# Performance work log

Measured on AMD Instinct MI355X. Metric: run time of the kernel, lower is better.

## Reference

```python
import jax, jax.numpy as jnp
import numpy as np

EMB = 16
L = 100
B = 8192
BN_EPS = 1e-5


def _bn(x, g, b):
    # BatchNorm1d in training mode: biased batch stats over dim 0. x: [b, EMB]
    mu = jnp.mean(x, axis=0)
    var = jnp.mean((x - mu) ** 2, axis=0)
    return g * (x - mu) / jnp.sqrt(var + BN_EPS) + b


def _pool(me, aw, g6, b6, a6):
    # me: [b, L, EMB] masked embeddings; aw: [b, L, 1] masked attention logits
    s = jnp.sum(me, axis=1)                       # sum pool
    mean = jnp.mean(me, axis=1)                   # mean over full L (incl. padding), as in torch
    sq = me * me
    l2 = jnp.sum(sq, axis=-1)                     # [b, L]
    mx_i = jnp.argmax(l2, axis=1)                 # first max, matches torch.max
    mn_i = jnp.argmin(jnp.where(l2 == 0, jnp.asarray(9999.0, l2.dtype), l2), axis=1)
    mx = jnp.take_along_axis(me, mx_i[:, None, None], axis=1)[:, 0]
    mn = jnp.take_along_axis(me, mn_i[:, None, None], axis=1)[:, 0]
    attw = jax.nn.softmax(aw, axis=1)             # softmax over L incl. zeroed pads (faithful)
    at = jnp.sum(me * attw, axis=1)
    ko = 0.5 * (s * s - jnp.sum(sq, axis=1))      # korder (FM-style)
    ko = ko / jnp.maximum(jnp.linalg.norm(ko, axis=-1, keepdims=True), 1e-12)
    # branch order: sum, mean, max, min, korder, atten (matches torch.cat order)
    pools = jnp.stack([
        _bn(s, g6[0], b6[0]), _bn(mean, g6[1], b6[1]), _bn(mx, g6[2], b6[2]),
        _bn(mn, g6[3], b6[3]), _bn(ko, g6[4], b6[4]), _bn(at, g6[5], b6[5])], axis=1)
    w = jax.nn.softmax(a6)[None, :, None]
    return jnp.sum(pools * w, axis=1)             # [b, EMB]


def setup_inputs() -> dict:
    key = jax.random.key(0)
    ks = jax.random.split(key, 24)
    f32 = jnp.float32
    inp = {
        'uid': jax.random.randint(ks[0], (B,), 0, 139000),
        'mid': jax.random.randint(ks[1], (B,), 0, 132000),
        'yr': jax.random.randint(ks[2], (B,), 0, 150),
        'ids_ug': jax.random.randint(ks[3], (B, L), 0, 30),
        'ids_urb': jax.random.randint(ks[4], (B, L), 0, 132000),
        'ids_mg': jax.random.randint(ks[5], (B, L), 0, 30),
        'ids_mt': jax.random.randint(ks[6], (B, L), 0, 41000),
        'len_ug': jax.random.randint(ks[7], (B,), 1, L + 1),
        'len_urb': jax.random.randint(ks[8], (B,), 1, L + 1),
        'len_mg': jax.random.randint(ks[9], (B,), 1, L + 1),
        'len_mt': jax.random.randint(ks[10], (B,), 1, L + 1),
        'emb_userId': jax.random.normal(ks[11], (139000, EMB), f32) * 0.05,
        'emb_movieId': jax.random.normal(ks[12], (132000, EMB), f32) * 0.05,
        'emb_tagId': jax.random.normal(ks[13], (41000, EMB), f32) * 0.05,
        'emb_genreId': jax.random.normal(ks[14], (30, EMB), f32) * 0.05,
        'emb_year': jax.random.normal(ks[15], (150, EMB), f32) * 0.05,
        # init_param(): atten embeddings ~ N(1.0, 1e-6)
        'att_movieId': 1.0 + jax.random.normal(ks[16], (132000, 1), f32) * 1e-6,
        'att_tagId': 1.0 + jax.random.normal(ks[17], (41000, 1), f32) * 1e-6,
        'att_genreId': 1.0 + jax.random.normal(ks[18], (30, 1), f32) * 1e-6,
        'bn_gamma': jnp.ones((4, 6, EMB), f32),
        'bn_beta': jnp.zeros((4, 6, EMB), f32),
        'alpha': jnp.ones((4, 6), f32),
        'W1': jax.random.normal(ks[19], (112, 64), f32) * 0.05,
        'b1': jnp.zeros((64,), f32),
        'W2': jax.random.normal(ks[20], (64, 32), f32) * 0.05,
        'b2': jnp.zeros((32,), f32),
        'W3': jax.random.normal(ks[21], (32, 1), f32) * 0.05,
        'b3': jnp.zeros((1,), f32),
    }
    return inp


def reference(uid, mid, yr, ids_ug, ids_urb, ids_mg, ids_mt,
              len_ug, len_urb, len_mg, len_mt,
              emb_userId, emb_movieId, emb_tagId, emb_genreId, emb_year,
              att_movieId, att_tagId, att_genreId,
              bn_gamma, bn_beta, alpha, W1, b1, W2, b2, W3, b3):
    emb1 = jnp.concatenate([emb_userId[uid], emb_movieId[mid], emb_year[yr]], axis=1)  # [b, 48]
    ar = jnp.arange(L)
    fields = [
        (ids_ug, len_ug, emb_genreId, att_genreId),
        (ids_urb, len_urb, emb_movieId, att_movieId),
        (ids_mg, len_mg, emb_genreId, att_genreId),
        (ids_mt, len_mt, emb_tagId, att_tagId),
    ]
    pooled = []
    for i, (ids, ln, tab, atab) in enumerate(fields):
        m = (ln[:, None] > ar)[..., None].astype(tab.dtype)  # [b, L, 1]
        me = tab[ids] * m
        aw = atab[ids] * m
        pooled.append(_pool(me, aw, bn_gamma[i], bn_beta[i], alpha[i]))
    x = jnp.concatenate([emb1] + pooled, axis=1)  # [b, 112]
    h = jax.nn.relu(x @ W1 + b1)
    h = jax.nn.relu(h @ W2 + b2)
    return jax.nn.sigmoid(h @ W3 + b3)[:, 0]
```

## Files before the change

kernel.cpp:

```cpp
#include <hip/hip_runtime.h>
#include <math.h>

#define BATCH 8192
#define L 100
#define EMB 16
#define NCH 384
#define NG  512

#define POOLED_FLOATS (4 * BATCH * 96)
#define POOLED_BYTES  (POOLED_FLOATS * 4)
#define PART_FLOATS   (NCH * NG)

__global__ __launch_bounds__(256) void pool_kernel(
    const int* __restrict__ ids_ug, const int* __restrict__ ids_urb,
    const int* __restrict__ ids_mg, const int* __restrict__ ids_mt,
    const int* __restrict__ len_ug, const int* __restrict__ len_urb,
    const int* __restrict__ len_mg, const int* __restrict__ len_mt,
    const float* __restrict__ emb_movie, const float* __restrict__ emb_tag,
    const float* __restrict__ emb_genre,
    const float* __restrict__ att_movie, const float* __restrict__ att_tag,
    const float* __restrict__ att_genre,
    float* __restrict__ pooled, float* __restrict__ psum, float* __restrict__ psq)
{
    const int bx  = blockIdx.x;
    const int f   = bx & 3;
    const int g   = bx >> 2;
    const int tid = threadIdx.x;
    const int sub = tid >> 4;
    const int e   = tid & 15;
    const int j   = e >> 2;
    const int c   = e & 3;
    const int b   = g * 16 + sub;

    const int* ids; const int* lens; const float* tab; const float* atab;
    switch (f) {
        case 0: ids = ids_ug;  lens = len_ug;  tab = emb_genre; atab = att_genre; break;
        case 1: ids = ids_urb; lens = len_urb; tab = emb_movie; atab = att_movie; break;
        case 2: ids = ids_mg;  lens = len_mg;  tab = emb_genre; atab = att_genre; break;
        default:ids = ids_mt;  lens = len_mt;  tab = emb_tag;   atab = att_tag;   break;
    }
    const int ln = lens[b];
    const float4* __restrict__ tab4 = (const float4*)tab;

    __shared__ float tile[16][100];
    __shared__ int   sids[16 * 100];
    __shared__ float gtab[480];
    __shared__ float gexp[32];

    {
        const int4* idsrc = (const int4*)(ids + (size_t)g * (16 * L));
        ((int4*)sids)[tid]       = idsrc[tid];
        if (tid < 144) ((int4*)sids)[256 + tid] = idsrc[256 + tid];
    }
    const bool genre = (f == 0) | (f == 2);
    if (genre) {
        for (int i = tid; i < 480; i += 256) gtab[i] = emb_genre[i];
        if (tid < 30) gexp[tid] = __expf(att_genre[tid]);
    }
    __syncthreads();
    const int* idrow = &sids[sub * 100];

    float4 s   = make_float4(0.f, 0.f, 0.f, 0.f);
    float4 ssq = s, att = s, mxv = s, mnv = s;
    float expsum = 0.f;
    float bestmx = -1e30f; int lx = 0x7fffffff;
    float bestmn =  1e30f; int lm = 0x7fffffff;

    auto ACC = [&](const float4 v, const float ew, const int l) {
        float4 v2;
        v2.x = v.x * v.x; v2.y = v.y * v.y; v2.z = v.z * v.z; v2.w = v.w * v.w;
        s.x += v.x; s.y += v.y; s.z += v.z; s.w += v.w;
        ssq.x += v2.x; ssq.y += v2.y; ssq.z += v2.z; ssq.w += v2.w;
        float pl2 = (v2.x + v2.y) + (v2.z + v2.w);
        float l2 = pl2 + __shfl_xor(pl2, 1);
        l2 += __shfl_xor(l2, 2);
        if (l2 > bestmx) { bestmx = l2; lx = l; mxv = v; }
        float l2m = (l2 == 0.0f) ? 9999.0f : l2;
        if (l2m < bestmn) { bestmn = l2m; lm = l; mnv = v; }
        expsum += ew;
        att.x += v.x * ew; att.y += v.y * ew; att.z += v.z * ew; att.w += v.w * ew;
    };

    if (!genre) {
        int l = j;
        if (l < ln) {
            int id0 = idrow[l];
            float4 v0 = tab4[(size_t)id0 * 4 + c];
            float aw0 = atab[id0];
            while (l + 4 < ln) {
                const int id1 = idrow[l + 4];
                float4 v1 = tab4[(size_t)id1 * 4 + c];
                float aw1 = atab[id1];
                ACC(v0, __expf(aw0), l);
                v0 = v1; aw0 = aw1; l += 4;
            }
            ACC(v0, __expf(aw0), l);
        }
    } else {
        for (int l = j; l < ln; l += 4) {
            const int id = idrow[l];
            float4 v = *(const float4*)&gtab[id * 16 + c * 4];
            ACC(v, gexp[id], l);
        }
    }

    #pragma unroll
    for (int m = 4; m <= 8; m <<= 1) {
        float obx = __shfl_xor(bestmx, m);
        int   olx = __shfl_xor(lx, m);
        float ax = __shfl_xor(mxv.x, m), ay = __shfl_xor(mxv.y, m);
        float az = __shfl_xor(mxv.z, m), aw2 = __shfl_xor(mxv.w, m);
        if (obx > bestmx || (obx == bestmx && olx < lx)) {
            bestmx = obx; lx = olx; mxv = make_float4(ax, ay, az, aw2);
        }
        float obn = __shfl_xor(bestmn, m);
        int   olm = __shfl_xor(lm, m);
        float bx2 = __shfl_xor(mnv.x, m), by = __shfl_xor(mnv.y, m);
        float bz  = __shfl_xor(mnv.z, m), bw = __shfl_xor(mnv.w, m);
        if (obn < bestmn || (obn == bestmn && olm < lm)) {
            bestmn = obn; lm = olm; mnv = make_float4(bx2, by, bz, bw);
        }
        s.x += __shfl_xor(s.x, m); s.y += __shfl_xor(s.y, m);
        s.z += __shfl_xor(s.z, m); s.w += __shfl_xor(s.w, m);
        ssq.x += __shfl_xor(ssq.x, m); ssq.y += __shfl_xor(ssq.y, m);
        ssq.z += __shfl_xor(ssq.z, m); ssq.w += __shfl_xor(ssq.w, m);
        att.x += __shfl_xor(att.x, m); att.y += __shfl_xor(att.y, m);
        att.z += __shfl_xor(att.z, m); att.w += __shfl_xor(att.w, m);
        expsum += __shfl_xor(expsum, m);
    }
    expsum += (float)(L - ln);

    float4 mean;
    mean.x = s.x * (1.0f / L); mean.y = s.y * (1.0f / L);
    mean.z = s.z * (1.0f / L); mean.w = s.w * (1.0f / L);
    float4 ko;
    ko.x = 0.5f * (s.x * s.x - ssq.x); ko.y = 0.5f * (s.y * s.y - ssq.y);
    ko.z = 0.5f * (s.z * s.z - ssq.z); ko.w = 0.5f * (s.w * s.w - ssq.w);
    float pk = (ko.x * ko.x + ko.y * ko.y) + (ko.z * ko.z + ko.w * ko.w);
    float kn2 = pk + __shfl_xor(pk, 1);
    kn2 += __shfl_xor(kn2, 2);
    float rn = 1.0f / fmaxf(sqrtf(kn2), 1e-12f);
    ko.x *= rn; ko.y *= rn; ko.z *= rn; ko.w *= rn;
    float ie = 1.0f / expsum;
    att.x *= ie; att.y *= ie; att.z *= ie; att.w *= ie;

    float4 pv[6] = { s, mean, mxv, mnv, ko, att };

    float4* prow = (float4*)(pooled + ((size_t)(f * BATCH + b)) * 96);
    if (j == 0) {
        #pragma unroll
        for (int p = 0; p < 6; ++p) {
            prow[p * 4 + c] = pv[p];
            *(float4*)&tile[sub][p * 16 + c * 4] = pv[p];
        }
    }
    __syncthreads();
    if (tid < 96) {
        float sm = 0.f, sq = 0.f;
        #pragma unroll
        for (int s2 = 0; s2 < 16; ++s2) {
            float x = tile[s2][tid];
            sm += x;
            sq += x * x;
        }
        psum[(size_t)(f * 96 + tid) * NG + g] = sm;
        psq [(size_t)(f * 96 + tid) * NG + g] = sq;
    }
}

__global__ __launch_bounds__(256) void coef_kernel(
    const float* __restrict__ psum, const float* __restrict__ psq,
    const float* __restrict__ gamma, const float* __restrict__ beta,
    const float* __restrict__ alpha,
    float* __restrict__ coefA, float* __restrict__ coefB)
{
    const int tid   = threadIdx.x;
    const int chl   = tid >> 3;
    const int strip = tid & 7;
    const int ch    = blockIdx.x * 32 + chl;
    const float4* ps = (const float4*)(psum + (size_t)ch * NG + strip * 64);
    const float4* pq = (const float4*)(psq  + (size_t)ch * NG + strip * 64);
    double dsm = 0.0, dsq = 0.0;
    #pragma unroll
    for (int i = 0; i < 16; ++i) {
        float4 a = ps[i];
        dsm += ((double)a.x + (double)a.y) + ((double)a.z + (double)a.w);
        float4 bq = pq[i];
        dsq += ((double)bq.x + (double)bq.y) + ((double)bq.z + (double)bq.w);
    }
    #pragma unroll
    for (int m = 1; m <= 4; m <<= 1) {
        dsm += __shfl_xor(dsm, m);
        dsq += __shfl_xor(dsq, m);
    }
    if (strip == 0) {
        const int f = ch / 96;
        const int p = (ch % 96) >> 4;
        double mu  = dsm * (1.0 / BATCH);
        double var = dsq * (1.0 / BATCH) - mu * mu;
        float inv = (float)(1.0 / sqrt(var + 1e-5));
        float gm = gamma[ch];
        float bb = beta[ch];
        float amax = -1e30f;
        for (int q = 0; q < 6; ++q) amax = fmaxf(amax, alpha[f * 6 + q]);
        float wsum = 0.f;
        for (int q = 0; q < 6; ++q) wsum += __expf(alpha[f * 6 + q] - amax);
        float wp = __expf(alpha[f * 6 + p] - amax) / wsum;
        coefA[ch] = wp * gm * inv;
        coefB[ch] = wp * (bb - gm * (float)mu * inv);
    }
}

#define SPB 16
__global__ __launch_bounds__(256) void final_kernel(
    const int* __restrict__ uid, const int* __restrict__ mid, const int* __restrict__ yr,
    const float* __restrict__ emb_user, const float* __restrict__ emb_movie,
    const float* __restrict__ emb_year,
    const float* __restrict__ pooled,
    const float* __restrict__ coefA, const float* __restrict__ coefB,
    const float* __restrict__ W1, const float* __restrict__ b1,
    const float* __restrict__ W2, const float* __restrict__ b2,
    const float* __restrict__ W3, const float* __restrict__ b3,
    float* __restrict__ out)
{
    __shared__ float sW1[112 * 64];
    __shared__ float sW2[64 * 32];
    __shared__ float sW3[32];
    __shared__ float sb1[64];
    __shared__ float sb2[32];
    __shared__ float xt[SPB][112];
    __shared__ float h1t[SPB][64];

    const int tid = threadIdx.x;
    for (int i = tid; i < 112 * 16; i += 256)
        ((float4*)sW1)[i] = ((const float4*)W1)[i];
    for (int i = tid; i < 64 * 8; i += 256)
        ((float4*)sW2)[i] = ((const float4*)W2)[i];
    if (tid < 32) sW3[tid] = W3[tid];
    if (tid < 64) sb1[tid] = b1[tid];
    if (tid < 32) sb2[tid] = b2[tid];

    const int sub = tid >> 4;
    const int e   = tid & 15;
    const int b   = blockIdx.x * SPB + sub;

    xt[sub][e]      = emb_user [(size_t)uid[b] * EMB + e];
    xt[sub][16 + e] = emb_movie[(size_t)mid[b] * EMB + e];
    xt[sub][32 + e] = emb_year [(size_t)yr[b]  * EMB + e];

    #pragma unroll
    for (int f = 0; f < 4; ++f) {
        const float* pr = pooled + ((size_t)(f * BATCH + b)) * 96;
        float acc = 0.f;
        #pragma unroll
        for (int p = 0; p < 6; ++p) {
            int c = f * 96 + p * 16 + e;
            acc += coefA[c] * pr[p * 16 + e] + coefB[c];
        }
        xt[sub][48 + f * 16 + e] = acc;
    }
    __syncthreads();

    float4 h1 = ((float4*)sb1)[e];
    for (int k = 0; k < 112; ++k) {
        float xk = xt[sub][k];
        float4 w = ((float4*)sW1)[k * 16 + e];
        h1.x += xk * w.x; h1.y += xk * w.y; h1.z += xk * w.z; h1.w += xk * w.w;
    }
    float4 h1r;
    h1r.x = fmaxf(h1.x, 0.f); h1r.y = fmaxf(h1.y, 0.f);
    h1r.z = fmaxf(h1.z, 0.f); h1r.w = fmaxf(h1.w, 0.f);
    *(float4*)&h1t[sub][e * 4] = h1r;
    __syncthreads();

    float2 h2 = ((float2*)sb2)[e];
    for (int k = 0; k < 64; ++k) {
        float hk = h1t[sub][k];
        float2 w = ((float2*)sW2)[k * 16 + e];
        h2.x += hk * w.x; h2.y += hk * w.y;
    }
    float part = fmaxf(h2.x, 0.f) * sW3[2 * e] + fmaxf(h2.y, 0.f) * sW3[2 * e + 1];
    part += __shfl_xor(part, 1);
    part += __shfl_xor(part, 2);
    part += __shfl_xor(part, 4);
    part += __shfl_xor(part, 8);
    if (e == 0) {
        float t = part + b3[0];
        out[b] = 1.f / (1.f + __expf(-t));
    }
}

extern "C" void kernel_launch(void* const* d_in, const int* in_sizes, int n_in,
                              void* d_out, int out_size, void* d_ws, size_t ws_size,
                              hipStream_t stream) {
    const int* uid     = (const int*)d_in[0];
    const int* mid     = (const int*)d_in[1];
    const int* yr      = (const int*)d_in[2];
    const int* ids_ug  = (const int*)d_in[3];
    const int* ids_urb = (const int*)d_in[4];
    const int* ids_mg  = (const int*)d_in[5];
    const int* ids_mt  = (const int*)d_in[6];
    const int* len_ug  = (const int*)d_in[7];
    const int* len_urb = (const int*)d_in[8];
    const int* len_mg  = (const int*)d_in[9];
    const int* len_mt  = (const int*)d_in[10];
    const float* emb_user  = (const float*)d_in[11];
    const float* emb_movie = (const float*)d_in[12];
    const float* emb_tag   = (const float*)d_in[13];
    const float* emb_genre = (const float*)d_in[14];
    const float* emb_year  = (const float*)d_in[15];
    const float* att_movie = (const float*)d_in[16];
    const float* att_tag   = (const float*)d_in[17];
    const float* att_genre = (const float*)d_in[18];
    const float* bn_gamma  = (const float*)d_in[19];
    const float* bn_beta   = (const float*)d_in[20];
    const float* alpha     = (const float*)d_in[21];
    const float* W1 = (const float*)d_in[22];
    const float* b1 = (const float*)d_in[23];
    const float* W2 = (const float*)d_in[24];
    const float* b2 = (const float*)d_in[25];
    const float* W3 = (const float*)d_in[26];
    const float* b3 = (const float*)d_in[27];
    float* out = (float*)d_out;

    float* pooled = (float*)d_ws;
    float* psum   = pooled + POOLED_FLOATS;
    float* psq    = psum + PART_FLOATS;
    float* coefA  = psq + PART_FLOATS;
    float* coefB  = coefA + NCH;

    pool_kernel<<<4 * NG, 256, 0, stream>>>(
        ids_ug, ids_urb, ids_mg, ids_mt,
        len_ug, len_urb, len_mg, len_mt,
        emb_movie, emb_tag, emb_genre,
        att_movie, att_tag, att_genre,
        pooled, psum, psq);
    coef_kernel<<<12, 256, 0, stream>>>(psum, psq, bn_gamma, bn_beta, alpha,
                                        coefA, coefB);
    final_kernel<<<BATCH / SPB, 256, 0, stream>>>(
        uid, mid, yr, emb_user, emb_movie, emb_year,
        pooled, coefA, coefB, W1, b1, W2, b2, W3, b3, out);
}
```

Measured before the change: 168.2 us.

## Interleave embedding rows with precomputed exp attention in a fused table

Adds a pre-pass kernel that copies the movie and tag embedding tables into a 128-byte-stride layout, with exp of the attention logit stored next to each row. The pool kernel then reads both embedding and attention weight from the same cache line and skips the per-element exp. This aims to cut the separate scattered attention gather. The cost is an extra kernel that rewrites roughly 173k rows, about 22 MB of writes, on every call.

```diff
diff --git a/kernel.cpp b/kernel.cpp
--- a/kernel.cpp
+++ b/kernel.cpp
@@ -6,20 +6,40 @@
 #define EMB 16
 #define NCH 384
 #define NG  512
+#define NM  132000
+#define NT  41000
 
 #define POOLED_FLOATS (4 * BATCH * 96)
-#define POOLED_BYTES  (POOLED_FLOATS * 4)
 #define PART_FLOATS   (NCH * NG)
+
+
+__global__ __launch_bounds__(256) void fuse_kernel(
+    const float* __restrict__ emb_m, const float* __restrict__ att_m,
+    const float* __restrict__ emb_t, const float* __restrict__ att_t,
+    float* __restrict__ fm, float* __restrict__ ft)
+{
+    const int t   = blockIdx.x * 256 + threadIdx.x;
+    const int row = t >> 2;
+    const int c   = t & 3;
+    if (row < NM) {
+        float4 v = ((const float4*)emb_m)[(size_t)row * 4 + c];
+        ((float4*)fm)[(size_t)row * 8 + c] = v;
+        if (c == 0) fm[(size_t)row * 32 + 16] = __expf(att_m[row]);
+    } else if (row < NM + NT) {
+        const int r = row - NM;
+        float4 v = ((const float4*)emb_t)[(size_t)r * 4 + c];
+        ((float4*)ft)[(size_t)r * 8 + c] = v;
+        if (c == 0) ft[(size_t)r * 32 + 16] = __expf(att_t[r]);
+    }
+}
 
 __global__ __launch_bounds__(256) void pool_kernel(
     const int* __restrict__ ids_ug, const int* __restrict__ ids_urb,
     const int* __restrict__ ids_mg, const int* __restrict__ ids_mt,
     const int* __restrict__ len_ug, const int* __restrict__ len_urb,
     const int* __restrict__ len_mg, const int* __restrict__ len_mt,
-    const float* __restrict__ emb_movie, const float* __restrict__ emb_tag,
-    const float* __restrict__ emb_genre,
-    const float* __restrict__ att_movie, const float* __restrict__ att_tag,
-    const float* __restrict__ att_genre,
+    const float* __restrict__ fm, const float* __restrict__ ft,
+    const float* __restrict__ emb_genre, const float* __restrict__ att_genre,
     float* __restrict__ pooled, float* __restrict__ psum, float* __restrict__ psq)
 {
     const int bx  = blockIdx.x;
@@ -32,15 +52,14 @@
     const int c   = e & 3;
     const int b   = g * 16 + sub;
 
-    const int* ids; const int* lens; const float* tab; const float* atab;
+    const int* ids; const int* lens; const float* ftab = nullptr;
     switch (f) {
-        case 0: ids = ids_ug;  lens = len_ug;  tab = emb_genre; atab = att_genre; break;
-        case 1: ids = ids_urb; lens = len_urb; tab = emb_movie; atab = att_movie; break;
-        case 2: ids = ids_mg;  lens = len_mg;  tab = emb_genre; atab = att_genre; break;
-        default:ids = ids_mt;  lens = len_mt;  tab = emb_tag;   atab = att_tag;   break;
+        case 0: ids = ids_ug;  lens = len_ug;  break;
+        case 1: ids = ids_urb; lens = len_urb; ftab = fm; break;
+        case 2: ids = ids_mg;  lens = len_mg;  break;
+        default:ids = ids_mt;  lens = len_mt;  ftab = ft; break;
     }
     const int ln = lens[b];
-    const float4* __restrict__ tab4 = (const float4*)tab;
 
     __shared__ float tile[16][100];
     __shared__ int   sids[16 * 100];
@@ -82,19 +101,20 @@
     };
 
     if (!genre) {
+        const float4* ftab4 = (const float4*)ftab;
         int l = j;
         if (l < ln) {
             int id0 = idrow[l];
-            float4 v0 = tab4[(size_t)id0 * 4 + c];
-            float aw0 = atab[id0];
+            float4 v0 = ftab4[(size_t)id0 * 8 + c];
+            float ew0 = ftab[(size_t)id0 * 32 + 16];
             while (l + 4 < ln) {
                 const int id1 = idrow[l + 4];
-                float4 v1 = tab4[(size_t)id1 * 4 + c];
-                float aw1 = atab[id1];
-                ACC(v0, __expf(aw0), l);
-                v0 = v1; aw0 = aw1; l += 4;
+                float4 v1 = ftab4[(size_t)id1 * 8 + c];
+                float ew1 = ftab[(size_t)id1 * 32 + 16];
+                ACC(v0, ew0, l);
+                v0 = v1; ew0 = ew1; l += 4;
             }
-            ACC(v0, __expf(aw0), l);
+            ACC(v0, ew0, l);
         }
     } else {
         for (int l = j; l < ln; l += 4) {
@@ -328,12 +348,21 @@
     float* psq    = psum + PART_FLOATS;
     float* coefA  = psq + PART_FLOATS;
     float* coefB  = coefA + NCH;
-
+    float* fusedM = coefB + NCH;
+    float* fusedT = fusedM + (size_t)NM * 32;
+
+    {
+        const int jobs   = (NM + NT) * 4;
+        const int blocks = (jobs + 255) / 256;
+        fuse_kernel<<<blocks, 256, 0, stream>>>(emb_movie, att_movie,
+                                                emb_tag, att_tag,
+                                                fusedM, fusedT);
+    }
     pool_kernel<<<4 * NG, 256, 0, stream>>>(
         ids_ug, ids_urb, ids_mg, ids_mt,
         len_ug, len_urb, len_mg, len_mt,
-        emb_movie, emb_tag, emb_genre,
-        att_movie, att_tag, att_genre,
+        fusedM, fusedT,
+        emb_genre, att_genre,
         pooled, psum, psq);
     coef_kernel<<<12, 256, 0, stream>>>(psum, psq, bn_gamma, bn_beta, alpha,
                                         coefA, coefB);
```

After: 176.7 us. 1.05x slower.
